# Performance work log

Measured on AMD Instinct MI355X. Metric: run time of the kernel, lower is better.

The kernel has to match this reference:

```python
import jax, jax.numpy as jnp
import numpy as np

D_MODEL = 1024
HEADS = 8
WINDOW = 64
N_PATCH = 512
N_TOK = 512
TEXT_D = 768
IMAGE_D = 1024
B = 1


def _sliding_window_attn(x, ctx, qw, qb, kw, kb, vw, vb, ow, ob, window, heads):
    # Faithful to the torch loop: window i covers context[max(0,i-w//2) : min(T,i+w//2+1)+1],
    # i.e. up to w+2 real tokens; zero-padded (unmasked!) up to w tokens when shorter.
    B_, N, Dm = x.shape
    T = ctx.shape[1]
    L = window + 2
    dh = Dm // heads
    q = x @ qw.T + qb  # (B,N,D)
    idx = jnp.arange(N)[:, None] + (jnp.arange(L) - window // 2)[None, :]  # (N,L)
    valid = (idx >= 0) & (idx < T)                      # real context tokens
    length = valid.sum(-1)                              # real tokens per window
    n_zero = jnp.maximum(0, window - length)            # zero-pad count (torch pads to w)
    inv_rank = jnp.cumsum(~valid, axis=-1) - 1          # rank among invalid slots
    attend = valid | ((~valid) & (inv_rank < n_zero[:, None]))  # real + zero-pad slots
    ctxw = jnp.where(valid[None, :, :, None], ctx[:, jnp.clip(idx, 0, T - 1), :], 0.0)  # (B,N,L,D)
    k = ctxw @ kw.T + kb                                # bias hits zero-pad slots too (as torch)
    v = ctxw @ vw.T + vb
    qh = q.reshape(B_, N, heads, dh)
    kh = k.reshape(B_, N, L, heads, dh)
    vh = v.reshape(B_, N, L, heads, dh)
    s = jnp.einsum('bnhd,bnlhd->bhnl', qh, kh) / jnp.sqrt(jnp.asarray(dh, x.dtype))
    s = jnp.where(attend[None, None], s, jnp.asarray(-1e9, x.dtype))
    a = jax.nn.softmax(s, axis=-1)
    o = jnp.einsum('bhnl,bnlhd->bnhd', a, vh).reshape(B_, N, Dm)
    return o @ ow.T + ob + x  # residual add, as in torch loop


def setup_inputs() -> dict:
    key = jax.random.key(0)
    ks = jax.random.split(key, 32)
    s = 0.02
    inp = {
        'images': jax.random.normal(ks[0], (B, N_PATCH, IMAGE_D), jnp.float32),
        'capitions': jax.random.normal(ks[1], (B, N_TOK, TEXT_D), jnp.float32),
        'text_input_ids': jax.random.randint(ks[2], (B, N_TOK), 0, 32000, jnp.int64)
        if jax.config.jax_enable_x64 else jax.random.randint(ks[2], (B, N_TOK), 0, 32000, jnp.int32),
        'tp_w': jax.random.normal(ks[3], (D_MODEL, TEXT_D), jnp.float32) * s,
        'tp_b': jnp.zeros((D_MODEL,), jnp.float32),
        'ip_w': jax.random.normal(ks[4], (D_MODEL, IMAGE_D), jnp.float32) * s,
        'ip_b': jnp.zeros((D_MODEL,), jnp.float32),
    }
    names = ['qw', 'kw', 'vw', 'ow']
    i = 5
    for pre in ['ia_', 'ta_']:
        for n in names:
            inp[pre + n] = jax.random.normal(ks[i], (D_MODEL, D_MODEL), jnp.float32) * s
            inp[pre + n[0] + 'b'] = jnp.zeros((D_MODEL,), jnp.float32)
            i += 1
    return inp


def reference(images, capitions, text_input_ids,
              tp_w, tp_b, ip_w, ip_b,
              ia_qw, ia_qb, ia_kw, ia_kb, ia_vw, ia_vb, ia_ow, ia_ob,
              ta_qw, ta_qb, ta_kw, ta_kb, ta_vw, ta_vb, ta_ow, ta_ob):
    txt = capitions @ tp_w.T + tp_b   # (B,Ntok,D)
    img = images @ ip_w.T + ip_b      # (B,Npatch,D)
    fused_img = _sliding_window_attn(img, txt, ia_qw, ia_qb, ia_kw, ia_kb,
                                     ia_vw, ia_vb, ia_ow, ia_ob, WINDOW, HEADS)
    fused_txt = _sliding_window_attn(txt, img, ta_qw, ta_qb, ta_kw, ta_kb,
                                     ta_vw, ta_vb, ta_ow, ta_ob, WINDOW, HEADS)
    return fused_img, fused_txt
```

## Files before the change

### kernel.cpp

```cpp
#include <hip/hip_runtime.h>
#include <hip/hip_bf16.h>

#define MDIM 512
#define NDIM 1024
#define LSLOT 66

typedef __attribute__((ext_vector_type(8))) short short8;
typedef __attribute__((ext_vector_type(4))) float f32x4;

struct GDesc {
    const float* A;
    const float* W;
    const float* bias;
    const float* res;
    float* C;
    int K;
};
struct GBatch { GDesc d[6]; };

static __device__ __forceinline__ short f2bf(float f) {
    return __builtin_bit_cast(short, __float2bfloat16(f));
}
static __device__ __forceinline__ short8 cvt8(float4 a, float4 b) {
    short8 v;
    v[0] = f2bf(a.x); v[1] = f2bf(a.y); v[2] = f2bf(a.z); v[3] = f2bf(a.w);
    v[4] = f2bf(b.x); v[5] = f2bf(b.y); v[6] = f2bf(b.z); v[7] = f2bf(b.w);
    return v;
}

__global__ __launch_bounds__(256) void gemm_mfma(GBatch gb) {
    GDesc g = gb.d[blockIdx.z];
    const int K = g.K;
    __shared__ __align__(16) short lds[2][2][64 * 64];

    const int tid  = threadIdx.x;
    const int lane = tid & 63;
    const int wave = tid >> 6;
    const int wm = (wave >> 1) * 32;
    const int wn = (wave & 1) * 32;
    const int m0 = blockIdx.y * 64;
    const int n0 = blockIdx.x * 64;

    const int srow = tid >> 2;
    const int sk   = (tid & 3) * 16;
    const int e0 = (sk >> 3);
    const int sidx0 = srow * 64 + ((e0 ^ (srow & 7)) << 3);
    const int sidx1 = srow * 64 + (((e0 + 1) ^ (srow & 7)) << 3);
    const float* gA = g.A + (size_t)(m0 + srow) * K + sk;
    const float* gW = g.W + (size_t)(n0 + srow) * K + sk;

    const int fr = lane & 15;
    const int fq = lane >> 4;

    f32x4 acc[2][2] = {};
    const int NT = K / 64;

    {
        float4 a0 = *(const float4*)gA,       a1 = *(const float4*)(gA + 4);
        float4 a2 = *(const float4*)(gA + 8), a3 = *(const float4*)(gA + 12);
        float4 w0 = *(const float4*)gW,       w1 = *(const float4*)(gW + 4);
        float4 w2 = *(const float4*)(gW + 8), w3 = *(const float4*)(gW + 12);
        *(short8*)&lds[0][0][sidx0] = cvt8(a0, a1);
        *(short8*)&lds[0][0][sidx1] = cvt8(a2, a3);
        *(short8*)&lds[0][1][sidx0] = cvt8(w0, w1);
        *(short8*)&lds[0][1][sidx1] = cvt8(w2, w3);
    }
    __syncthreads();

    int buf = 0;
    for (int t = 0; t < NT; ++t) {
        float4 a0, a1, a2, a3, w0, w1, w2, w3;
        const bool more = (t + 1 < NT);
        if (more) {
            const float* pa = gA + (t + 1) * 64;
            const float* pw = gW + (t + 1) * 64;
            a0 = *(const float4*)pa;       a1 = *(const float4*)(pa + 4);
            a2 = *(const float4*)(pa + 8); a3 = *(const float4*)(pa + 12);
            w0 = *(const float4*)pw;       w1 = *(const float4*)(pw + 4);
            w2 = *(const float4*)(pw + 8); w3 = *(const float4*)(pw + 12);
        }

        short8 af[2][2], wf[2][2];
#pragma unroll
        for (int i = 0; i < 2; ++i) {
            const int r = wm + i * 16 + fr;
            const int c = wn + i * 16 + fr;
#pragma unroll
            for (int kk = 0; kk < 2; ++kk) {
                const int sa = ((kk * 4 + fq) ^ (fr & 7)) << 3;
                af[i][kk] = *(short8*)&lds[buf][0][r * 64 + sa];
                wf[i][kk] = *(short8*)&lds[buf][1][c * 64 + sa];
            }
        }
#pragma unroll
        for (int kk = 0; kk < 2; ++kk)
#pragma unroll
            for (int i = 0; i < 2; ++i)
#pragma unroll
                for (int j = 0; j < 2; ++j)
                    acc[i][j] = __builtin_amdgcn_mfma_f32_16x16x32_bf16(
                        af[i][kk], wf[j][kk], acc[i][j], 0, 0, 0);

        if (more) {
            *(short8*)&lds[buf ^ 1][0][sidx0] = cvt8(a0, a1);
            *(short8*)&lds[buf ^ 1][0][sidx1] = cvt8(a2, a3);
            *(short8*)&lds[buf ^ 1][1][sidx0] = cvt8(w0, w1);
            *(short8*)&lds[buf ^ 1][1][sidx1] = cvt8(w2, w3);
        }
        __syncthreads();
        buf ^= 1;
    }

#pragma unroll
    for (int i = 0; i < 2; ++i) {
#pragma unroll
        for (int j = 0; j < 2; ++j) {
            const int col = n0 + wn + j * 16 + (lane & 15);
            const float b = g.bias[col];
            const int row0 = m0 + wm + i * 16 + (lane >> 4) * 4;
#pragma unroll
            for (int r = 0; r < 4; ++r) {
                float v = acc[i][j][r] + b;
                if (g.res) v += g.res[(size_t)(row0 + r) * NDIM + col];
                g.C[(size_t)(row0 + r) * NDIM + col] = v;
            }
        }
    }
}

struct AttnArgs {
    const float *Q, *K, *V, *kb, *vb;
    float* O;
};

__global__ __launch_bounds__(256) void attn_tile(AttnArgs a0, AttnArgs a1) {
    const AttnArgs a = blockIdx.z ? a1 : a0;
    const int h  = blockIdx.y;
    const int n0 = blockIdx.x * 32;
    const int tid = threadIdx.x;

    __shared__ float Ks[97 * 128];
    __shared__ float Vs[97 * 128];
    __shared__ float Qs[32 * 132];
    __shared__ float Ps[32 * 68];
    __shared__ float InvS[32];

    for (int i = tid; i < 97 * 32; i += 256) {
        const int wp = i >> 5, d4 = i & 31;
        const int idx = n0 - 32 + wp;
        const bool valid = (idx >= 0) && (idx < MDIM);
        const float* sk = (valid ? (a.K + (size_t)idx * NDIM) : a.kb) + h * 128;
        const float* sv = (valid ? (a.V + (size_t)idx * NDIM) : a.vb) + h * 128;
        const float4 kv = *(const float4*)(sk + d4 * 4);
        const float4 vv = *(const float4*)(sv + d4 * 4);
        const int slot = d4 ^ (wp & 31);
        *(float4*)&Ks[wp * 128 + slot * 4] = kv;
        *(float4*)&Vs[wp * 128 + slot * 4] = vv;
    }
    for (int i = tid; i < 32 * 32; i += 256) {
        const int r = i >> 5, d4 = i & 31;
        *(float4*)&Qs[r * 132 + d4 * 4] =
            *(const float4*)(a.Q + (size_t)(n0 + r) * NDIM + h * 128 + d4 * 4);
    }
    __syncthreads();

    const int r = tid >> 3, sub = tid & 7;
    const int n = n0 + r;
    const int lo_inv = max(0, 32 - n);
    const int hi_inv = max(0, n - 478);
    const int n_zero = max(0, 64 - (LSLOT - lo_inv - hi_inv));
    const float scale = 0.088388347648318447f;

    float dots[9];
#pragma unroll
    for (int k = 0; k < 9; ++k) dots[k] = 0.f;
#pragma unroll
    for (int db = 0; db < 4; ++db) {
        float4 q[8];
#pragma unroll
        for (int c = 0; c < 8; ++c) q[c] = *(float4*)&Qs[r * 132 + (db * 8 + c) * 4];
        for (int k = 0; k < 9; ++k) {
            const int l = sub + 8 * k;
            if (l >= LSLOT) break;
            const int wp = r + l, key = wp & 31;
            float accd = dots[k];
#pragma unroll
            for (int c = 0; c < 8; ++c) {
                const int d4 = db * 8 + c;
                const float4 kv = *(float4*)&Ks[wp * 128 + (d4 ^ key) * 4];
                accd += kv.x * q[c].x + kv.y * q[c].y + kv.z * q[c].z + kv.w * q[c].w;
            }
            dots[k] = accd;
        }
    }
    for (int k = 0; k < 9; ++k) {
        const int l = sub + 8 * k;
        if (l >= LSLOT) break;
        const int idx = n - 32 + l;
        const bool valid = (idx >= 0) && (idx < MDIM);
        bool attend = valid;
        if (!valid) {
            const int ir = (l < lo_inv) ? l : (l - (LSLOT - hi_inv));
            attend = ir < n_zero;
        }
        Ps[r * 68 + l] = attend ? dots[k] * scale : -1e30f;
    }
    __syncthreads();

    {
        float m = -1e30f;
        for (int k = 0; k < 9; ++k) {
            const int l = sub + 8 * k;
            if (l < LSLOT) m = fmaxf(m, Ps[r * 68 + l]);
        }
        for (int s = 1; s < 8; s <<= 1) m = fmaxf(m, __shfl_xor(m, s, 64));
        float sum = 0.f;
        for (int k = 0; k < 9; ++k) {
            const int l = sub + 8 * k;
            if (l >= LSLOT) break;
            const float e = expf(Ps[r * 68 + l] - m);
            Ps[r * 68 + l] = e;
            sum += e;
        }
        for (int s = 1; s < 8; s <<= 1) sum += __shfl_xor(sum, s, 64);
        if (sub == 0) InvS[r] = 1.0f / sum;
    }
    __syncthreads();

    float4 acc[4] = {};
    for (int l = 0; l < LSLOT; ++l) {
        const float p = Ps[r * 68 + l];
        const int wp = r + l, key = wp & 31;
#pragma unroll
        for (int c = 0; c < 4; ++c) {
            const int d4 = sub + 8 * c;
            const float4 vv = *(float4*)&Vs[wp * 128 + (d4 ^ key) * 4];
            acc[c].x += p * vv.x; acc[c].y += p * vv.y;
            acc[c].z += p * vv.z; acc[c].w += p * vv.w;
        }
    }
    const float inv = InvS[r];
#pragma unroll
    for (int c = 0; c < 4; ++c) {
        float4 v = acc[c];
        v.x *= inv; v.y *= inv; v.z *= inv; v.w *= inv;
        *(float4*)(a.O + (size_t)n * NDIM + h * 128 + (sub + 8 * c) * 4) = v;
    }
}

extern "C" void kernel_launch(void* const* d_in, const int* in_sizes, int n_in,
                              void* d_out, int out_size, void* d_ws, size_t ws_size,
                              hipStream_t stream) {
    const float* images = (const float*)d_in[0];
    const float* caps   = (const float*)d_in[1];
    const float* tp_w = (const float*)d_in[3];
    const float* tp_b = (const float*)d_in[4];
    const float* ip_w = (const float*)d_in[5];
    const float* ip_b = (const float*)d_in[6];
    const float* ia_qw = (const float*)d_in[7];  const float* ia_qb = (const float*)d_in[8];
    const float* ia_kw = (const float*)d_in[9];  const float* ia_kb = (const float*)d_in[10];
    const float* ia_vw = (const float*)d_in[11]; const float* ia_vb = (const float*)d_in[12];
    const float* ia_ow = (const float*)d_in[13]; const float* ia_ob = (const float*)d_in[14];
    const float* ta_qw = (const float*)d_in[15]; const float* ta_qb = (const float*)d_in[16];
    const float* ta_kw = (const float*)d_in[17]; const float* ta_kb = (const float*)d_in[18];
    const float* ta_vw = (const float*)d_in[19]; const float* ta_vb = (const float*)d_in[20];
    const float* ta_ow = (const float*)d_in[21]; const float* ta_ob = (const float*)d_in[22];

    const size_t S = (size_t)MDIM * NDIM;
    float* ws = (float*)d_ws;
    float* txt = ws + 0 * S;
    float* img = ws + 1 * S;
    float* Qi  = ws + 2 * S;
    float* Ki  = ws + 3 * S;
    float* Vi  = ws + 4 * S;
    float* Qt  = ws + 5 * S;
    float* Kt  = ws + 6 * S;
    float* Vt  = ws + 7 * S;
    float* Oi  = ws + 8 * S;
    float* Ot  = ws + 9 * S;

    float* fused_img = (float*)d_out;
    float* fused_txt = (float*)d_out + S;

    dim3 blk(256);
    dim3 tiles(NDIM / 64, MDIM / 64);

    GBatch b1 = {};
    b1.d[0] = {caps,   tp_w, tp_b, nullptr, txt, 768};
    b1.d[1] = {images, ip_w, ip_b, nullptr, img, 1024};
    gemm_mfma<<<dim3(tiles.x, tiles.y, 2), blk, 0, stream>>>(b1);

    GBatch b2 = {};
    b2.d[0] = {img, ia_qw, ia_qb, nullptr, Qi, 1024};
    b2.d[1] = {txt, ia_kw, ia_kb, nullptr, Ki, 1024};
    b2.d[2] = {txt, ia_vw, ia_vb, nullptr, Vi, 1024};
    b2.d[3] = {txt, ta_qw, ta_qb, nullptr, Qt, 1024};
    b2.d[4] = {img, ta_kw, ta_kb, nullptr, Kt, 1024};
    b2.d[5] = {img, ta_vw, ta_vb, nullptr, Vt, 1024};
    gemm_mfma<<<dim3(tiles.x, tiles.y, 6), blk, 0, stream>>>(b2);

    AttnArgs aa = {Qi, Ki, Vi, ia_kb, ia_vb, Oi};
    AttnArgs ab = {Qt, Kt, Vt, ta_kb, ta_vb, Ot};
    attn_tile<<<dim3(16, 8, 2), blk, 0, stream>>>(aa, ab);

    GBatch b4 = {};
    b4.d[0] = {Oi, ia_ow, ia_ob, img, fused_img, 1024};
    b4.d[1] = {Ot, ta_ow, ta_ob, txt, fused_txt, 1024};
    gemm_mfma<<<dim3(tiles.x, tiles.y, 2), blk, 0, stream>>>(b4);
}
```

Measured before the change: 209.6 us.

## Pre-convert operands to bf16 and stream GEMM tiles via direct global-to-LDS loads

Adds a batched conversion kernel that turns inputs and all weight matrices into bf16 once per call. GEMMs then read bf16 through global_load_lds straight into swizzled LDS, with 128-thread blocks where one wave loads A and one loads W. The first GEMM also writes bf16 copies of txt/img, and attention writes its output in bf16, which halves GEMM input traffic and removes in-loop conversion. The cost is an extra kernel pass that converts about 10M floats each call, including weights, plus lower block occupancy.

```diff
diff --git a/kernel.cpp b/kernel.cpp
--- a/kernel.cpp
+++ b/kernel.cpp
@@ -6,17 +6,9 @@
 #define LSLOT 66
 
 typedef __attribute__((ext_vector_type(8))) short short8;
+typedef __attribute__((ext_vector_type(4))) short short4v;
 typedef __attribute__((ext_vector_type(4))) float f32x4;
-
-struct GDesc {
-    const float* A;
-    const float* W;
-    const float* bias;
-    const float* res;
-    float* C;
-    int K;
-};
-struct GBatch { GDesc d[6]; };
+typedef __hip_bfloat16 bf16;
 
 static __device__ __forceinline__ short f2bf(float f) {
     return __builtin_bit_cast(short, __float2bfloat16(f));
@@ -28,7 +20,36 @@
     return v;
 }
 
-__global__ __launch_bounds__(256) void gemm_mfma(GBatch gb) {
+static __device__ __forceinline__ void gload16(const void* g, void* l) {
+    __builtin_amdgcn_global_load_lds(
+        (const __attribute__((address_space(1))) unsigned int*)g,
+        (__attribute__((address_space(3))) unsigned int*)l, 16, 0, 0);
+}
+
+struct CvtDesc { const float* src; bf16* dst; int n; };
+struct CvtBatch { CvtDesc d[12]; };
+
+__global__ __launch_bounds__(256) void cvt_bf16(CvtBatch cb) {
+    CvtDesc c = cb.d[blockIdx.z];
+    const int i = (blockIdx.x * 256 + threadIdx.x) * 8;
+    if (i >= c.n) return;
+    const float4 a = *(const float4*)(c.src + i);
+    const float4 b = *(const float4*)(c.src + i + 4);
+    *(short8*)((short*)c.dst + i) = cvt8(a, b);
+}
+
+struct GDesc {
+    const bf16* A;
+    const bf16* W;
+    const float* bias;
+    const float* res;
+    float* C;
+    bf16* Cb;
+    int K;
+};
+struct GBatch { GDesc d[6]; };
+
+__global__ __launch_bounds__(128) void gemm_bf16(GBatch gb) {
     GDesc g = gb.d[blockIdx.z];
     const int K = g.K;
     __shared__ __align__(16) short lds[2][2][64 * 64];
@@ -36,93 +57,78 @@
     const int tid  = threadIdx.x;
     const int lane = tid & 63;
     const int wave = tid >> 6;
-    const int wm = (wave >> 1) * 32;
-    const int wn = (wave & 1) * 32;
     const int m0 = blockIdx.y * 64;
     const int n0 = blockIdx.x * 64;
-
-    const int srow = tid >> 2;
-    const int sk   = (tid & 3) * 16;
-    const int e0 = (sk >> 3);
-    const int sidx0 = srow * 64 + ((e0 ^ (srow & 7)) << 3);
-    const int sidx1 = srow * 64 + (((e0 + 1) ^ (srow & 7)) << 3);
-    const float* gA = g.A + (size_t)(m0 + srow) * K + sk;
-    const float* gW = g.W + (size_t)(n0 + srow) * K + sk;
+    const int wm = wave * 32;
+
+    const size_t rowb = (size_t)K * 2;
+    const char* sbase = (const char*)(wave ? (const void*)g.W : (const void*)g.A)
+                      + (size_t)(wave ? n0 : m0) * rowb
+                      + (size_t)(lane >> 3) * rowb
+                      + (size_t)(((lane & 7) ^ (lane >> 3)) << 4);
 
     const int fr = lane & 15;
     const int fq = lane >> 4;
 
-    f32x4 acc[2][2] = {};
+    f32x4 acc[2][4] = {};
     const int NT = K / 64;
 
-    {
-        float4 a0 = *(const float4*)gA,       a1 = *(const float4*)(gA + 4);
-        float4 a2 = *(const float4*)(gA + 8), a3 = *(const float4*)(gA + 12);
-        float4 w0 = *(const float4*)gW,       w1 = *(const float4*)(gW + 4);
-        float4 w2 = *(const float4*)(gW + 8), w3 = *(const float4*)(gW + 12);
-        *(short8*)&lds[0][0][sidx0] = cvt8(a0, a1);
-        *(short8*)&lds[0][0][sidx1] = cvt8(a2, a3);
-        *(short8*)&lds[0][1][sidx0] = cvt8(w0, w1);
-        *(short8*)&lds[0][1][sidx1] = cvt8(w2, w3);
-    }
+#pragma unroll
+    for (int i = 0; i < 8; ++i)
+        gload16(sbase + (size_t)i * 8 * rowb, &lds[0][wave][i * 512]);
     __syncthreads();
 
     int buf = 0;
     for (int t = 0; t < NT; ++t) {
-        float4 a0, a1, a2, a3, w0, w1, w2, w3;
-        const bool more = (t + 1 < NT);
-        if (more) {
-            const float* pa = gA + (t + 1) * 64;
-            const float* pw = gW + (t + 1) * 64;
-            a0 = *(const float4*)pa;       a1 = *(const float4*)(pa + 4);
-            a2 = *(const float4*)(pa + 8); a3 = *(const float4*)(pa + 12);
-            w0 = *(const float4*)pw;       w1 = *(const float4*)(pw + 4);
-            w2 = *(const float4*)(pw + 8); w3 = *(const float4*)(pw + 12);
-        }
-
-        short8 af[2][2], wf[2][2];
-#pragma unroll
-        for (int i = 0; i < 2; ++i) {
-            const int r = wm + i * 16 + fr;
-            const int c = wn + i * 16 + fr;
-#pragma unroll
-            for (int kk = 0; kk < 2; ++kk) {
-                const int sa = ((kk * 4 + fq) ^ (fr & 7)) << 3;
-                af[i][kk] = *(short8*)&lds[buf][0][r * 64 + sa];
-                wf[i][kk] = *(short8*)&lds[buf][1][c * 64 + sa];
+        if (t + 1 < NT) {
+            const char* p = sbase + (size_t)(t + 1) * 128;
+#pragma unroll
+            for (int i = 0; i < 8; ++i)
+                gload16(p + (size_t)i * 8 * rowb, &lds[buf ^ 1][wave][i * 512]);
+        }
+
+        short8 af[2][2], wf[4][2];
+#pragma unroll
+        for (int kk = 0; kk < 2; ++kk) {
+            const int ch = kk * 4 + fq;
+#pragma unroll
+            for (int i = 0; i < 2; ++i) {
+                const int r = wm + i * 16 + fr;
+                af[i][kk] = *(const short8*)&lds[buf][0][r * 64 + ((ch ^ (r & 7)) << 3)];
             }
+#pragma unroll
+            for (int j = 0; j < 4; ++j) {
+                const int c = j * 16 + fr;
+                wf[j][kk] = *(const short8*)&lds[buf][1][c * 64 + ((ch ^ (c & 7)) << 3)];
+            }
         }
 #pragma unroll
         for (int kk = 0; kk < 2; ++kk)
 #pragma unroll
             for (int i = 0; i < 2; ++i)
 #pragma unroll
-                for (int j = 0; j < 2; ++j)
+                for (int j = 0; j < 4; ++j)
                     acc[i][j] = __builtin_amdgcn_mfma_f32_16x16x32_bf16(
                         af[i][kk], wf[j][kk], acc[i][j], 0, 0, 0);
 
-        if (more) {
-            *(short8*)&lds[buf ^ 1][0][sidx0] = cvt8(a0, a1);
-            *(short8*)&lds[buf ^ 1][0][sidx1] = cvt8(a2, a3);
-            *(short8*)&lds[buf ^ 1][1][sidx0] = cvt8(w0, w1);
-            *(short8*)&lds[buf ^ 1][1][sidx1] = cvt8(w2, w3);
-        }
         __syncthreads();
         buf ^= 1;
     }
 
 #pragma unroll
     for (int i = 0; i < 2; ++i) {
-#pragma unroll
-        for (int j = 0; j < 2; ++j) {
-            const int col = n0 + wn + j * 16 + (lane & 15);
+        const int row0 = m0 + wm + i * 16 + fq * 4;
+#pragma unroll
+        for (int j = 0; j < 4; ++j) {
+            const int col = n0 + j * 16 + fr;
             const float b = g.bias[col];
-            const int row0 = m0 + wm + i * 16 + (lane >> 4) * 4;
 #pragma unroll
             for (int r = 0; r < 4; ++r) {
                 float v = acc[i][j][r] + b;
-                if (g.res) v += g.res[(size_t)(row0 + r) * NDIM + col];
-                g.C[(size_t)(row0 + r) * NDIM + col] = v;
+                const size_t o = (size_t)(row0 + r) * NDIM + col;
+                if (g.res) v += g.res[o];
+                g.C[o] = v;
+                if (g.Cb) g.Cb[o] = __float2bfloat16(v);
             }
         }
     }
@@ -130,7 +136,7 @@
 
 struct AttnArgs {
     const float *Q, *K, *V, *kb, *vb;
-    float* O;
+    bf16* O;
 };
 
 __global__ __launch_bounds__(256) void attn_tile(AttnArgs a0, AttnArgs a1) {
@@ -242,9 +248,10 @@
     const float inv = InvS[r];
 #pragma unroll
     for (int c = 0; c < 4; ++c) {
-        float4 v = acc[c];
-        v.x *= inv; v.y *= inv; v.z *= inv; v.w *= inv;
-        *(float4*)(a.O + (size_t)n * NDIM + h * 128 + (sub + 8 * c) * 4) = v;
+        short4v o;
+        o[0] = f2bf(acc[c].x * inv); o[1] = f2bf(acc[c].y * inv);
+        o[2] = f2bf(acc[c].z * inv); o[3] = f2bf(acc[c].w * inv);
+        *(short4v*)((short*)a.O + (size_t)n * NDIM + h * 128 + (sub + 8 * c) * 4) = o;
     }
 }
 
@@ -276,35 +283,60 @@
     float* Qt  = ws + 5 * S;
     float* Kt  = ws + 6 * S;
     float* Vt  = ws + 7 * S;
-    float* Oi  = ws + 8 * S;
-    float* Ot  = ws + 9 * S;
+    bf16* bb     = (bf16*)(ws + 8 * S);
+    bf16* capsb  = bb;
+    bf16* imgsb  = capsb + 393216;
+    bf16* txtb   = imgsb + S;
+    bf16* imgb   = txtb + S;
+    bf16* Oib    = imgb + S;
+    bf16* Otb    = Oib + S;
+    bf16* tp_wb  = Otb + S;
+    bf16* ip_wb  = tp_wb + 786432;
+    bf16* qwb[8];
+    { bf16* p = ip_wb + 1048576;
+      for (int i = 0; i < 8; ++i) { qwb[i] = p; p += 1048576; } }
 
     float* fused_img = (float*)d_out;
     float* fused_txt = (float*)d_out + S;
 
-    dim3 blk(256);
+    CvtBatch cv = {};
+    cv.d[0]  = {caps,   capsb, 393216};
+    cv.d[1]  = {images, imgsb, (int)S};
+    cv.d[2]  = {tp_w,   tp_wb, 786432};
+    cv.d[3]  = {ip_w,   ip_wb, 1048576};
+    cv.d[4]  = {ia_qw, qwb[0], 1048576};
+    cv.d[5]  = {ia_kw, qwb[1], 1048576};
+    cv.d[6]  = {ia_vw, qwb[2], 1048576};
+    cv.d[7]  = {ia_ow, qwb[3], 1048576};
+    cv.d[8]  = {ta_qw, qwb[4], 1048576};
+    cv.d[9]  = {ta_kw, qwb[5], 1048576};
+    cv.d[10] = {ta_vw, qwb[6], 1048576};
+    cv.d[11] = {ta_ow, qwb[7], 1048576};
+    cvt_bf16<<<dim3(512, 1, 12), 256, 0, stream>>>(cv);
+
+    dim3 blk(128);
     dim3 tiles(NDIM / 64, MDIM / 64);
 
     GBatch b1 = {};
-    b1.d[0] = {caps,   tp_w, tp_b, nullptr, txt, 768};
-    b1.d[1] = {images, ip_w, ip_b, nullptr, img, 1024};
-    gemm_mfma<<<dim3(tiles.x, tiles.y, 2), blk, 0, stream>>>(b1);
+    b1.d[0] = {capsb, tp_wb, tp_b, nullptr, txt, txtb, 768};
+    b1.d[1] = {imgsb, ip_wb, ip_b, nullptr, img, imgb, 1024};
+    gemm_bf16<<<dim3(tiles.x, tiles.y, 2), blk, 0, stream>>>(b1);
 
     GBatch b2 = {};
-    b2.d[0] = {img, ia_qw, ia_qb, nullptr, Qi, 1024};
-    b2.d[1] = {txt, ia_kw, ia_kb, nullptr, Ki, 1024};
-    b2.d[2] = {txt, ia_vw, ia_vb, nullptr, Vi, 1024};
-    b2.d[3] = {txt, ta_qw, ta_qb, nullptr, Qt, 1024};
-    b2.d[4] = {img, ta_kw, ta_kb, nullptr, Kt, 1024};
-    b2.d[5] = {img, ta_vw, ta_vb, nullptr, Vt, 1024};
-    gemm_mfma<<<dim3(tiles.x, tiles.y, 6), blk, 0, stream>>>(b2);
-
-    AttnArgs aa = {Qi, Ki, Vi, ia_kb, ia_vb, Oi};
-    AttnArgs ab = {Qt, Kt, Vt, ta_kb, ta_vb, Ot};
-    attn_tile<<<dim3(16, 8, 2), blk, 0, stream>>>(aa, ab);
+    b2.d[0] = {imgb, qwb[0], ia_qb, nullptr, Qi, nullptr, 1024};
+    b2.d[1] = {txtb, qwb[1], ia_kb, nullptr, Ki, nullptr, 1024};
+    b2.d[2] = {txtb, qwb[2], ia_vb, nullptr, Vi, nullptr, 1024};
+    b2.d[3] = {txtb, qwb[4], ta_qb, nullptr, Qt, nullptr, 1024};
+    b2.d[4] = {imgb, qwb[5], ta_kb, nullptr, Kt, nullptr, 1024};
+    b2.d[5] = {imgb, qwb[6], ta_vb, nullptr, Vt, nullptr, 1024};
+    gemm_bf16<<<dim3(tiles.x, tiles.y, 6), blk, 0, stream>>>(b2);
+
+    AttnArgs aa = {Qi, Ki, Vi, ia_kb, ia_vb, Oib};
+    AttnArgs ab = {Qt, Kt, Vt, ta_kb, ta_vb, Otb};
+    attn_tile<<<dim3(16, 8, 2), 256, 0, stream>>>(aa, ab);
 
     GBatch b4 = {};
-    b4.d[0] = {Oi, ia_ow, ia_ob, img, fused_img, 1024};
-    b4.d[1] = {Ot, ta_ow, ta_ob, txt, fused_txt, 1024};
-    gemm_mfma<<<dim3(tiles.x, tiles.y, 2), blk, 0, stream>>>(b4);
-}
+    b4.d[0] = {Oib, qwb[3], ia_ob, img, fused_img, nullptr, 1024};
+    b4.d[1] = {Otb, qwb[7], ta_ob, txt, fused_txt, nullptr, 1024};
+    gemm_bf16<<<dim3(tiles.x, tiles.y, 2), blk, 0, stream>>>(b4);
+}
```

Measured after the change: 186.8 us. 1.12x faster.
